# Kernel optimization log

Measured on AMD Instinct MI355X. Metric: run time of the kernel, lower is better.

Reference implementation:

```python
import jax, jax.numpy as jnp
import numpy as np

THR = 0.5      # span-selection threshold
K_SUBJ = 16    # max subject/object spans kept per sentence (padded)
K_OBJ = 8      # max object spans kept per (subject, relation)

# Greedy threshold-based span pairing: for each start position i with
# start_prob>THR, take the first unused j>=i with end_prob>THR (NMS-like).
# Returns fixed-size padded spans [K,2] (int32) and a validity mask [K].
def greedy_spans(sp, ep, K):
    S = sp.shape[0]
    idxs = jnp.arange(S, dtype=jnp.int32)
    def step(carry, i):
        used, count, spans, valid = carry
        gate = sp[i] > THR
        cand = (ep > THR) & (~used) & (idxs >= i)
        has = jnp.any(cand)
        j = jnp.argmax(cand).astype(jnp.int32)  # first True
        found = gate & has
        slot = jnp.minimum(count, K - 1)
        write = found & (count < K)
        pair = jnp.where(write, jnp.stack([i, j]).astype(jnp.int32), spans[slot])
        spans = spans.at[slot].set(pair)
        valid = valid.at[slot].set(valid[slot] | write)
        used = used.at[j].set(used[j] | found)
        count = count + found.astype(jnp.int32)
        return (used, count, spans, valid), None
    init = (jnp.zeros(S, bool), jnp.int32(0),
            jnp.zeros((K, 2), jnp.int32), jnp.zeros(K, bool))
    (_, _, spans, valid), _ = jax.lax.scan(step, init, idxs)
    return spans, valid


def _model(token_embs, hg, rel_embs, b_rel_transe, head_w, head_b,
           Wmats, Wbias, rproj_w, rproj_b, V_w, V_b):
    # head_w/head_b order: 0 start_subj, 1 end_subj, 2 b_start_obj, 3 b_end_obj,
    #                      4 start_obj, 5 end_obj, 6 b_start_subj, 7 b_end_subj
    # Wmats/Wbias order:   0 W_s, 1 W_r, 2 W_g, 3 W_x, 4 W_r_b, 5 W_g_b, 6 W_x_b, 7 W_x2
    sig = jax.nn.sigmoid
    head = lambda x, i: sig(x @ head_w[i] + head_b[i])        # H->1 sigmoid head
    lin = lambda x, i: x @ Wmats[i].T + Wbias[i]              # H->H linear

    # ---- first-level span scores + greedy extraction (forward & backward) ----
    sub_sp, sub_ep = head(token_embs, 0), head(token_embs, 1)   # [B,S]
    bob_sp, bob_ep = head(token_embs, 2), head(token_embs, 3)
    g = jax.vmap(lambda a, b: greedy_spans(a, b, K_SUBJ))
    subj_spans, subj_valid = g(sub_sp, sub_ep)                  # [B,K,2],[B,K]
    b_subj_spans, b_subj_valid = g(bob_sp, bob_ep)

    def gather(tok_b, spans, valid):  # mean of start/end token embeddings
        e = (tok_b[spans[:, 0]] + tok_b[spans[:, 1]]) * 0.5
        return e * valid[:, None].astype(tok_b.dtype)
    s_k = jax.vmap(gather)(token_embs, subj_spans, subj_valid)      # [B,K,H]
    b_s_k = jax.vmap(gather)(token_embs, b_subj_spans, b_subj_valid)
    s_k_w = lin(s_k, 0) * subj_valid[..., None]                     # W_s + mask
    b_s_k_w = lin(b_s_k, 0) * b_subj_valid[..., None]

    # ---- relation-aware attention context C = sum_s A[b,s,r] * x[b,s] ----
    b_rel = b_rel_transe @ rproj_w.T + rproj_b                      # r_proj
    def attend(rels, ir, ig, ix):
        e = jnp.tanh(lin(token_embs, ix)[:, :, None, :]             # [B,S,1,H]
                     + lin(hg, ig)[:, None, None, :]                # [B,1,1,H]
                     + lin(rels, ir)[None, None, :, :])             # [1,1,R,H]
        v = e @ V_w + V_b[0]                                        # [B,S,R]
        A = jax.nn.softmax(v, axis=1)                               # over seq
        return jnp.einsum('bsr,bsh->brh', A, token_embs)            # [B,R,H]
    C = attend(rel_embs, 1, 2, 3)
    b_C = attend(b_rel, 4, 5, 6)

    # Heads are linear, so distribute w over the sum instead of
    # materializing the [B,S,K,R,H] tensor.
    tok_mix = token_embs + lin(token_embs, 7)
    def pair_probs(Cmat, skw, i):
        t_tok = tok_mix @ head_w[i]                                 # [B,S]
        t_sub = skw @ head_w[i]                                     # [B,K]
        t_rel = Cmat @ head_w[i]                                    # [B,R]
        return sig(t_tok[:, :, None, None] + t_sub[:, None, :, None]
                   + t_rel[:, None, None, :] + head_b[i])           # [B,S,K,R]
    obj_sp, obj_ep = pair_probs(C, s_k_w, 4), pair_probs(C, s_k_w, 5)
    bsub_sp, bsub_ep = pair_probs(b_C, b_s_k_w, 6), pair_probs(b_C, b_s_k_w, 7)

    # ---- greedy object-span extraction per (batch, subject, relation) ----
    def triples(sp4, ep4, subj_ok):
        B_, S_, K_, R_ = sp4.shape
        fsp = sp4.transpose(0, 2, 3, 1).reshape(-1, S_)
        fep = ep4.transpose(0, 2, 3, 1).reshape(-1, S_)
        spans, valid = jax.vmap(lambda a, b: greedy_spans(a, b, K_OBJ))(fsp, fep)
        spans = spans.reshape(B_, K_, R_, K_OBJ, 2)
        valid = valid.reshape(B_, K_, R_, K_OBJ) & subj_ok[:, :, None, None]
        return spans, valid
    f_spans, f_valid = triples(obj_sp, obj_ep, subj_valid)
    bw_spans, bw_valid = triples(bsub_sp, bsub_ep, b_subj_valid)

    probs = jnp.stack([obj_sp, obj_ep, bsub_sp, bsub_ep])           # [4,B,S,K,R]
    return (probs, subj_spans, subj_valid, b_subj_spans, b_subj_valid,
            f_spans, f_valid, bw_spans, bw_valid)


def setup_inputs() -> dict:
    key = jax.random.key(0)
    ks = jax.random.split(key, 12)
    B, S, H, R, T = 8, 256, 768, 40, 80
    sc = H ** -0.5
    return {
        'token_embs': jax.random.normal(ks[0], (B, S, H), jnp.float32),
        'hg': jax.random.normal(ks[1], (B, H), jnp.float32),
        'rel_embs': jax.random.normal(ks[2], (R, H), jnp.float32),
        'b_rel_transe': jax.random.normal(ks[3], (R, T), jnp.float32),
        'head_w': jax.random.normal(ks[4], (8, H), jnp.float32) * sc,
        'head_b': jax.random.normal(ks[5], (8,), jnp.float32) * 0.1,
        'Wmats': jax.random.normal(ks[6], (8, H, H), jnp.float32) * sc,
        'Wbias': jax.random.normal(ks[7], (8, H), jnp.float32) * 0.02,
        'rproj_w': jax.random.normal(ks[8], (H, T), jnp.float32) * (T ** -0.5),
        'rproj_b': jax.random.normal(ks[9], (H,), jnp.float32) * 0.02,
        'V_w': jax.random.normal(ks[10], (H,), jnp.float32) * sc,
        'V_b': jax.random.normal(ks[11], (1,), jnp.float32) * 0.1,
    }


def reference(token_embs, hg, rel_embs, b_rel_transe, head_w, head_b,
              Wmats, Wbias, rproj_w, rproj_b, V_w, V_b):
    return _model(token_embs, hg, rel_embs, b_rel_transe, head_w, head_b,
                  Wmats, Wbias, rproj_w, rproj_b, V_w, V_b)
```

## Files before the change

kernel.cpp:

```cpp
#include <hip/hip_runtime.h>
#include <hip/hip_bf16.h>
#include <stdint.h>

#define Bc 8
#define Sc 256
#define Hc 768
#define Rc 40
#define Tc 80
#define KSc 16
#define KOc 8

#define OUT_SSP 5242880
#define OUT_SVA 5243136
#define OUT_BSP 5243264
#define OUT_BVA 5243520
#define OUT_FSP 5243648
#define OUT_FVA 5325568
#define OUT_WSP 5366528
#define OUT_WVA 5448448

#define CM_PS (16 * Rc * Hc)
#define BSH (Bc * Sc * Hc)

__device__ inline double wave_reduce_d(double v) {
#pragma unroll
  for (int o = 32; o; o >>= 1) v += __shfl_down(v, o, 64);
  return v;
}
__device__ inline float wave_reduce_f(float v) {
#pragma unroll
  for (int o = 32; o; o >>= 1) v += __shfl_down(v, o, 64);
  return v;
}

__global__ __launch_bounds__(256) void k_l03(const float* __restrict__ x,
                                             const float* __restrict__ head_w,
                                             const float* __restrict__ head_b,
                                             float* __restrict__ l03) {
  int bs = blockIdx.x * 4 + (threadIdx.x >> 6);
  int lane = threadIdx.x & 63;
  if (bs >= Bc * Sc) return;
  const float* xr = x + (size_t)bs * Hc;
  double acc[4] = {0.0, 0.0, 0.0, 0.0};
  for (int h = lane; h < Hc; h += 64) {
    double xv = (double)xr[h];
    acc[0] += xv * (double)head_w[h];
    acc[1] += xv * (double)head_w[Hc + h];
    acc[2] += xv * (double)head_w[2 * Hc + h];
    acc[3] += xv * (double)head_w[3 * Hc + h];
  }
#pragma unroll
  for (int i = 0; i < 4; ++i) {
    double a = wave_reduce_d(acc[i]);
    if (lane == 0) l03[i * (Bc * Sc) + bs] = (float)(a + (double)head_b[i]);
  }
}

__device__ inline int find_first(const uint64_t* epm, const uint64_t* used, int i) {
  int wi = i >> 6;
  uint64_t m = epm[wi] & ~used[wi] & (~0ull << (i & 63));
  if (m) return (wi << 6) + (__ffsll((unsigned long long)m) - 1);
  for (int w = wi + 1; w < 4; ++w) {
    uint64_t mm = epm[w] & ~used[w];
    if (mm) return (w << 6) + (__ffsll((unsigned long long)mm) - 1);
  }
  return -1;
}

__global__ __launch_bounds__(64) void k_greedy1(const float* __restrict__ l03,
                                                int* __restrict__ spans1, int* __restrict__ valid1,
                                                float* __restrict__ out) {
  int t = blockIdx.x;
  int dir = t >> 3, b = t & 7;
  int lane = threadIdx.x;
  const float* sp = l03 + (dir * 2) * (Bc * Sc) + b * Sc;
  const float* ep = sp + Bc * Sc;
  uint64_t spm[4], epm[4];
#pragma unroll
  for (int w = 0; w < 4; ++w) {
    spm[w] = __ballot(sp[w * 64 + lane] > 0.f);
    epm[w] = __ballot(ep[w * 64 + lane] > 0.f);
  }
  __shared__ int ssp0[KSc], ssp1[KSc], sva[KSc];
  if (lane < KSc) { ssp0[lane] = 0; ssp1[lane] = 0; sva[lane] = 0; }
  __syncthreads();
  if (lane == 0) {
    uint64_t used[4] = {0, 0, 0, 0};
    int cnt = 0;
#pragma unroll
    for (int w = 0; w < 4; ++w) {
      uint64_t g = spm[w];
      while (g) {
        int bit = __ffsll((unsigned long long)g) - 1;
        g &= g - 1;
        int i = w * 64 + bit;
        int j = find_first(epm, used, i);
        if (j < 0) continue;
        used[j >> 6] |= (1ull << (j & 63));
        if (cnt < KSc) { ssp0[cnt] = i; ssp1[cnt] = j; sva[cnt] = 1; }
        cnt++;
      }
    }
  }
  __syncthreads();
  int base = (dir * Bc + b) * KSc;
  float* osp = out + (dir ? OUT_BSP : OUT_SSP) + b * KSc * 2;
  float* ova = out + (dir ? OUT_BVA : OUT_SVA) + b * KSc;
  if (lane < KSc) {
    spans1[(base + lane) * 2] = ssp0[lane];
    spans1[(base + lane) * 2 + 1] = ssp1[lane];
    valid1[base + lane] = sva[lane];
    osp[lane * 2] = (float)ssp0[lane];
    osp[lane * 2 + 1] = (float)ssp1[lane];
    ova[lane] = (float)sva[lane];
  }
}

__global__ __launch_bounds__(256) void k_prep(const float* __restrict__ brt,
                                              const float* __restrict__ rw,
                                              const float* __restrict__ rb,
                                              const float* __restrict__ Wmats,
                                              const float* __restrict__ head_w,
                                              const float* __restrict__ x,
                                              const int* __restrict__ spans1,
                                              float* __restrict__ brel,
                                              double* __restrict__ hv,
                                              float* __restrict__ eb) {
  int bb = blockIdx.x;
  int tid = threadIdx.x;
  if (bb < 12) {
    int idx = bb * 256 + tid;
    int i = idx / Hc, j = idx % Hc;
    const float* h4 = head_w + (4 + i) * Hc;
    const float* W7 = Wmats + (size_t)7 * Hc * Hc;
    double acc = (double)h4[j];
    for (int hh = 0; hh < Hc; ++hh)
      acc += (double)W7[(size_t)hh * Hc + j] * (double)h4[hh];
    hv[idx] = acc;
  } else if (bb < 132) {
    int idx = (bb - 12) * 256 + tid;
    int r = idx / Hc, h = idx % Hc;
    float acc = rb[h];
    const float* a = brt + r * Tc;
    const float* w = rw + (size_t)h * Tc;
    for (int t = 0; t < Tc; ++t) acc = fmaf(a[t], w[t], acc);
    brel[idx] = acc;
  } else {
    int row = bb - 132;
    int b = (row / KSc) % Bc;
    int s0 = spans1[row * 2], s1 = spans1[row * 2 + 1];
    const float* x0 = x + ((size_t)b * Sc + s0) * Hc;
    const float* x1 = x + ((size_t)b * Sc + s1) * Hc;
    float* er = eb + (size_t)row * Hc;
    for (int h = tid; h < Hc; h += 256) er[h] = 0.5f * (x0[h] + x1[h]);
  }
}

__global__ __launch_bounds__(256) void k_skw(const float* __restrict__ eb,
                                             const float* __restrict__ Wmats,
                                             const float* __restrict__ Wbias,
                                             const int* __restrict__ valid1,
                                             float* __restrict__ skw) {
  int m0 = blockIdx.y * 32;
  int n0 = blockIdx.x * 64;
  __shared__ float Asl[32][36];
  __shared__ float Bsl[32][68];
  int tid = threadIdx.x;
  int arow = tid >> 3, acol = (tid & 7) << 2;
  int brow = tid >> 2, bcol = (tid & 3) << 2;
  int txi = tid & 15, tyi = tid >> 4;
  const float* ap = eb + (size_t)(m0 + arow) * Hc + acol;
  const float* bp = Wmats + (size_t)(n0 + brow) * Hc + bcol;
  int nb = n0 + txi * 4;
  float4 bias = *(const float4*)&Wbias[nb];
  float acc[2][4];
#pragma unroll
  for (int i = 0; i < 2; ++i) { acc[i][0] = bias.x; acc[i][1] = bias.y; acc[i][2] = bias.z; acc[i][3] = bias.w; }
  for (int k0 = 0; k0 < Hc; k0 += 32) {
    float4 av = *(const float4*)(ap + k0);
    float4 b0 = *(const float4*)(bp + k0);
    float4 b1 = *(const float4*)(bp + k0 + 16);
    __syncthreads();
    Asl[acol + 0][arow] = av.x; Asl[acol + 1][arow] = av.y; Asl[acol + 2][arow] = av.z; Asl[acol + 3][arow] = av.w;
    Bsl[bcol + 0][brow] = b0.x; Bsl[bcol + 1][brow] = b0.y; Bsl[bcol + 2][brow] = b0.z; Bsl[bcol + 3][brow] = b0.w;
    Bsl[bcol + 16][brow] = b1.x; Bsl[bcol + 17][brow] = b1.y; Bsl[bcol + 18][brow] = b1.z; Bsl[bcol + 19][brow] = b1.w;
    __syncthreads();
#pragma unroll
    for (int kk = 0; kk < 32; ++kk) {
      float a0 = Asl[kk][tyi * 2], a1 = Asl[kk][tyi * 2 + 1];
      float4 b = *(const float4*)&Bsl[kk][txi * 4];
      acc[0][0] = fmaf(a0, b.x, acc[0][0]); acc[0][1] = fmaf(a0, b.y, acc[0][1]);
      acc[0][2] = fmaf(a0, b.z, acc[0][2]); acc[0][3] = fmaf(a0, b.w, acc[0][3]);
      acc[1][0] = fmaf(a1, b.x, acc[1][0]); acc[1][1] = fmaf(a1, b.y, acc[1][1]);
      acc[1][2] = fmaf(a1, b.z, acc[1][2]); acc[1][3] = fmaf(a1, b.w, acc[1][3]);
    }
  }
  int m_ = m0 + tyi * 2;
#pragma unroll
  for (int i = 0; i < 2; ++i) {
    int v = valid1[m_ + i];
    float4 o;
    o.x = v ? acc[i][0] : 0.f; o.y = v ? acc[i][1] : 0.f;
    o.z = v ? acc[i][2] : 0.f; o.w = v ? acc[i][3] : 0.f;
    *(float4*)&skw[(size_t)(m_ + i) * Hc + nb] = o;
  }
}

__global__ __launch_bounds__(256) void k_tgtr(const float* __restrict__ hg,
                                              const float* __restrict__ rel,
                                              const float* __restrict__ brel,
                                              const float* __restrict__ Wmats,
                                              const float* __restrict__ Wbias,
                                              float* __restrict__ tg,
                                              float* __restrict__ tr) {
  int grp = blockIdx.z;
  const float* Asrc; int M; int wsel; float* dst;
  if (grp == 0)      { Asrc = hg;   M = 8;  wsel = 2; dst = tg; }
  else if (grp == 1) { Asrc = hg;   M = 8;  wsel = 5; dst = tg + 8 * Hc; }
  else if (grp == 2) { Asrc = rel;  M = 40; wsel = 1; dst = tr; }
  else               { Asrc = brel; M = 40; wsel = 4; dst = tr + 40 * Hc; }
  int m0 = blockIdx.y * 32;
  if (m0 >= M) return;
  int n0 = blockIdx.x * 64;
  const float* W = Wmats + (size_t)wsel * Hc * Hc;
  const float* bias = Wbias + wsel * Hc;
  __shared__ float Asl[32][36];
  __shared__ float Bsl[32][68];
  int tid = threadIdx.x;
  int arow = tid >> 3, acol = (tid & 7) << 2;
  int brow = tid >> 2, bcol = (tid & 3) << 2;
  int txi = tid & 15, tyi = tid >> 4;
  int ar = m0 + arow;
  const float* ap = Asrc + (size_t)(ar < M ? ar : 0) * Hc + acol;
  const float* bp = W + (size_t)(n0 + brow) * Hc + bcol;
  int nb = n0 + txi * 4;
  float4 bv = *(const float4*)&bias[nb];
  float acc[2][4];
#pragma unroll
  for (int i = 0; i < 2; ++i) { acc[i][0] = bv.x; acc[i][1] = bv.y; acc[i][2] = bv.z; acc[i][3] = bv.w; }
  for (int k0 = 0; k0 < Hc; k0 += 32) {
    float4 av = *(const float4*)(ap + k0);
    float4 b0 = *(const float4*)(bp + k0);
    float4 b1 = *(const float4*)(bp + k0 + 16);
    __syncthreads();
    Asl[acol + 0][arow] = av.x; Asl[acol + 1][arow] = av.y; Asl[acol + 2][arow] = av.z; Asl[acol + 3][arow] = av.w;
    Bsl[bcol + 0][brow] = b0.x; Bsl[bcol + 1][brow] = b0.y; Bsl[bcol + 2][brow] = b0.z; Bsl[bcol + 3][brow] = b0.w;
    Bsl[bcol + 16][brow] = b1.x; Bsl[bcol + 17][brow] = b1.y; Bsl[bcol + 18][brow] = b1.z; Bsl[bcol + 19][brow] = b1.w;
    __syncthreads();
#pragma unroll
    for (int kk = 0; kk < 32; ++kk) {
      float a0 = Asl[kk][tyi * 2], a1 = Asl[kk][tyi * 2 + 1];
      float4 b = *(const float4*)&Bsl[kk][txi * 4];
      acc[0][0] = fmaf(a0, b.x, acc[0][0]); acc[0][1] = fmaf(a0, b.y, acc[0][1]);
      acc[0][2] = fmaf(a0, b.z, acc[0][2]); acc[0][3] = fmaf(a0, b.w, acc[0][3]);
      acc[1][0] = fmaf(a1, b.x, acc[1][0]); acc[1][1] = fmaf(a1, b.y, acc[1][1]);
      acc[1][2] = fmaf(a1, b.z, acc[1][2]); acc[1][3] = fmaf(a1, b.w, acc[1][3]);
    }
  }
  int m_ = m0 + tyi * 2;
#pragma unroll
  for (int i = 0; i < 2; ++i) {
    if (m_ + i < M) {
      float4 o; o.x = acc[i][0]; o.y = acc[i][1]; o.z = acc[i][2]; o.w = acc[i][3];
      *(float4*)&dst[(size_t)(m_ + i) * Hc + nb] = o;
    }
  }
}

#define BM 64
#define BN 64
#define BKK 32
#define LDP 68
__global__ __launch_bounds__(256) void k_tx(const float* __restrict__ x,
                                            const float* __restrict__ Wmats,
                                            const float* __restrict__ Wbias,
                                            float* __restrict__ txo) {
  int dir = blockIdx.z;
  const float* W = Wmats + (size_t)(dir ? 6 : 3) * Hc * Hc;
  const float* bias = Wbias + (dir ? 6 : 3) * Hc;
  float* outp = txo + (size_t)dir * BSH;
  int m0 = blockIdx.y * BM;
  int n0 = blockIdx.x * BN;
  __shared__ float Asl[BKK][LDP];
  __shared__ float Bsl[BKK][LDP];
  int tid = threadIdx.x;
  int lr = tid >> 2;
  int lc = (tid & 3) << 2;
  int txi = tid & 15, tyi = tid >> 4;
  const float* xp = x + (size_t)(m0 + lr) * Hc + lc;
  const float* wp = W + (size_t)(n0 + lr) * Hc + lc;
  float4 a0 = *(const float4*)(xp);
  float4 a1 = *(const float4*)(xp + 16);
  float4 b0 = *(const float4*)(wp);
  float4 b1 = *(const float4*)(wp + 16);
  float acc[4][4] = {};
  for (int k0 = 0; k0 < Hc; k0 += BKK) {
    __syncthreads();
    Asl[lc + 0][lr] = a0.x; Asl[lc + 1][lr] = a0.y; Asl[lc + 2][lr] = a0.z; Asl[lc + 3][lr] = a0.w;
    Asl[lc + 16][lr] = a1.x; Asl[lc + 17][lr] = a1.y; Asl[lc + 18][lr] = a1.z; Asl[lc + 19][lr] = a1.w;
    Bsl[lc + 0][lr] = b0.x; Bsl[lc + 1][lr] = b0.y; Bsl[lc + 2][lr] = b0.z; Bsl[lc + 3][lr] = b0.w;
    Bsl[lc + 16][lr] = b1.x; Bsl[lc + 17][lr] = b1.y; Bsl[lc + 18][lr] = b1.z; Bsl[lc + 19][lr] = b1.w;
    __syncthreads();
    if (k0 + BKK < Hc) {
      a0 = *(const float4*)(xp + k0 + BKK);
      a1 = *(const float4*)(xp + k0 + BKK + 16);
      b0 = *(const float4*)(wp + k0 + BKK);
      b1 = *(const float4*)(wp + k0 + BKK + 16);
    }
#pragma unroll
    for (int kk = 0; kk < BKK; ++kk) {
      float4 a = *(const float4*)&Asl[kk][tyi * 4];
      float4 b = *(const float4*)&Bsl[kk][txi * 4];
      acc[0][0] = fmaf(a.x, b.x, acc[0][0]); acc[0][1] = fmaf(a.x, b.y, acc[0][1]);
      acc[0][2] = fmaf(a.x, b.z, acc[0][2]); acc[0][3] = fmaf(a.x, b.w, acc[0][3]);
      acc[1][0] = fmaf(a.y, b.x, acc[1][0]); acc[1][1] = fmaf(a.y, b.y, acc[1][1]);
      acc[1][2] = fmaf(a.y, b.z, acc[1][2]); acc[1][3] = fmaf(a.y, b.w, acc[1][3]);
      acc[2][0] = fmaf(a.z, b.x, acc[2][0]); acc[2][1] = fmaf(a.z, b.y, acc[2][1]);
      acc[2][2] = fmaf(a.z, b.z, acc[2][2]); acc[2][3] = fmaf(a.z, b.w, acc[2][3]);
      acc[3][0] = fmaf(a.w, b.x, acc[3][0]); acc[3][1] = fmaf(a.w, b.y, acc[3][1]);
      acc[3][2] = fmaf(a.w, b.z, acc[3][2]); acc[3][3] = fmaf(a.w, b.w, acc[3][3]);
    }
  }
  int nb = n0 + txi * 4;
  float4 bb = *(const float4*)&bias[nb];
#pragma unroll
  for (int i2 = 0; i2 < 4; ++i2) {
    float4 o;
    o.x = acc[i2][0] + bb.x; o.y = acc[i2][1] + bb.y;
    o.z = acc[i2][2] + bb.z; o.w = acc[i2][3] + bb.w;
    *(float4*)&outp[(size_t)(m0 + tyi * 4 + i2) * Hc + nb] = o;
  }
}

__global__ __launch_bounds__(256) void k_v(const float* __restrict__ txo,
                                           const float* __restrict__ tg,
                                           const float* __restrict__ tr,
                                           const float* __restrict__ Vw,
                                           const float* __restrict__ Vb,
                                           float* __restrict__ va) {
  const float Cl = 2.8853900817779268f;
  int id = blockIdx.x;
  int dir = id >> 10;
  int rem = id & 1023;
  int rhalf = rem & 1;
  int bs0 = (rem >> 1) * 4;
  int b = bs0 >> 8;
  int tid = threadIdx.x;
  int wv = tid >> 6, lane = tid & 63;
  const float* tgr = tg + (dir * Bc + b) * Hc;
  float xt[4][12], vw[12];
#pragma unroll
  for (int u = 0; u < 12; ++u) {
    int h = lane + 64 * u;
    vw[u] = Vw[h];
    float tgv = tgr[h];
#pragma unroll
    for (int si = 0; si < 4; ++si)
      xt[si][u] = (txo[((size_t)dir * (Bc * Sc) + bs0 + si) * Hc + h] + tgv) * Cl;
  }
  float vb0 = Vb[0];
  for (int q = 0; q < 5; ++q) {
    int r = rhalf * 20 + wv * 5 + q;
    const float* trr = tr + ((size_t)dir * Rc + r) * Hc + lane;
    float p0 = 0.f, p1 = 0.f, p2 = 0.f, p3 = 0.f;
#pragma unroll
    for (int u = 0; u < 12; ++u) {
      float t = trr[64 * u] * Cl;
      float e0 = __builtin_amdgcn_exp2f(xt[0][u] + t);
      float e1 = __builtin_amdgcn_exp2f(xt[1][u] + t);
      float e2 = __builtin_amdgcn_exp2f(xt[2][u] + t);
      float e3 = __builtin_amdgcn_exp2f(xt[3][u] + t);
      p0 = fmaf(fmaf(-2.f, __builtin_amdgcn_rcpf(e0 + 1.f), 1.f), vw[u], p0);
      p1 = fmaf(fmaf(-2.f, __builtin_amdgcn_rcpf(e1 + 1.f), 1.f), vw[u], p1);
      p2 = fmaf(fmaf(-2.f, __builtin_amdgcn_rcpf(e2 + 1.f), 1.f), vw[u], p2);
      p3 = fmaf(fmaf(-2.f, __builtin_amdgcn_rcpf(e3 + 1.f), 1.f), vw[u], p3);
    }
    p0 = wave_reduce_f(p0); p1 = wave_reduce_f(p1);
    p2 = wave_reduce_f(p2); p3 = wave_reduce_f(p3);
    if (lane == 0) {
      size_t base = ((size_t)dir * (Bc * Sc) + bs0) * Rc + r;
      va[base] = p0 + vb0;
      va[base + Rc] = p1 + vb0;
      va[base + 2 * Rc] = p2 + vb0;
      va[base + 3 * Rc] = p3 + vb0;
    }
  }
}

__global__ __launch_bounds__(256) void k_softmax(float* __restrict__ va) {
  int id = blockIdx.x;
  int dir = id / (Bc * Rc); int rem = id % (Bc * Rc);
  int b = rem / Rc; int r = rem % Rc;
  int s = threadIdx.x;
  float* base = va + (((size_t)dir * Bc + b) * Sc) * Rc + r;
  float v = base[(size_t)s * Rc];
  __shared__ float red[8];
  float m = v;
#pragma unroll
  for (int o = 32; o; o >>= 1) m = fmaxf(m, __shfl_xor(m, o, 64));
  if ((s & 63) == 0) red[s >> 6] = m;
  __syncthreads();
  if (s == 0) red[4] = fmaxf(fmaxf(red[0], red[1]), fmaxf(red[2], red[3]));
  __syncthreads();
  m = red[4];
  float e = expf(v - m);
  float t = e;
#pragma unroll
  for (int o = 32; o; o >>= 1) t += __shfl_xor(t, o, 64);
  __syncthreads();
  if ((s & 63) == 0) red[s >> 6] = t;
  __syncthreads();
  if (s == 0) red[4] = red[0] + red[1] + red[2] + red[3];
  __syncthreads();
  base[(size_t)s * Rc] = e / red[4];
}

__global__ __launch_bounds__(256, 1) void k_C(const float* __restrict__ va,
                                              const float* __restrict__ x,
                                              float* __restrict__ Cm4) {
  int id = blockIdx.x;
  int p = id & 3;
  int g = id >> 2;
  int b = g & 7;
  __shared__ float As_[64 * Rc];
  int tid = threadIdx.x;
  const float* vab = va + ((size_t)g * Sc + p * 64) * Rc;
  for (int idx = tid; idx < 64 * Rc; idx += 256) As_[idx] = vab[idx];
  __syncthreads();
  const float* xb = x + ((size_t)b * Sc + p * 64) * Hc;
  float acc[3][Rc];
#pragma unroll
  for (int j = 0; j < 3; ++j)
#pragma unroll
    for (int r = 0; r < Rc; ++r) acc[j][r] = 0.f;
  for (int s = 0; s < 64; ++s) {
    float xv0 = xb[(size_t)s * Hc + tid];
    float xv1 = xb[(size_t)s * Hc + 256 + tid];
    float xv2 = xb[(size_t)s * Hc + 512 + tid];
#pragma unroll
    for (int q = 0; q < 10; ++q) {
      float4 a4 = *(const float4*)&As_[s * Rc + q * 4];
      acc[0][q * 4 + 0] = fmaf(a4.x, xv0, acc[0][q * 4 + 0]);
      acc[0][q * 4 + 1] = fmaf(a4.y, xv0, acc[0][q * 4 + 1]);
      acc[0][q * 4 + 2] = fmaf(a4.z, xv0, acc[0][q * 4 + 2]);
      acc[0][q * 4 + 3] = fmaf(a4.w, xv0, acc[0][q * 4 + 3]);
      acc[1][q * 4 + 0] = fmaf(a4.x, xv1, acc[1][q * 4 + 0]);
      acc[1][q * 4 + 1] = fmaf(a4.y, xv1, acc[1][q * 4 + 1]);
      acc[1][q * 4 + 2] = fmaf(a4.z, xv1, acc[1][q * 4 + 2]);
      acc[1][q * 4 + 3] = fmaf(a4.w, xv1, acc[1][q * 4 + 3]);
      acc[2][q * 4 + 0] = fmaf(a4.x, xv2, acc[2][q * 4 + 0]);
      acc[2][q * 4 + 1] = fmaf(a4.y, xv2, acc[2][q * 4 + 1]);
      acc[2][q * 4 + 2] = fmaf(a4.z, xv2, acc[2][q * 4 + 2]);
      acc[2][q * 4 + 3] = fmaf(a4.w, xv2, acc[2][q * 4 + 3]);
    }
  }
#pragma unroll
  for (int r = 0; r < Rc; ++r) {
    size_t base = ((size_t)(p * 16 + g) * Rc + r) * Hc + tid;
    Cm4[base] = acc[0][r];
    Cm4[base + 256] = acc[1][r];
    Cm4[base + 512] = acc[2][r];
  }
}

__global__ __launch_bounds__(256) void k_tt(const float* __restrict__ x,
                                            const double* __restrict__ hv,
                                            double* __restrict__ tt) {
  int bs = blockIdx.x * 4 + (threadIdx.x >> 6);
  int lane = threadIdx.x & 63;
  if (bs >= Bc * Sc) return;
  const float* xr = x + (size_t)bs * Hc;
  double acc[4] = {0.0, 0.0, 0.0, 0.0};
  for (int h = lane; h < Hc; h += 64) {
    double xv = (double)xr[h];
    acc[0] += xv * hv[h];
    acc[1] += xv * hv[Hc + h];
    acc[2] += xv * hv[2 * Hc + h];
    acc[3] += xv * hv[3 * Hc + h];
  }
#pragma unroll
  for (int i = 0; i < 4; ++i) {
    double a = wave_reduce_d(acc[i]);
    if (lane == 0) tt[i * (Bc * Sc) + bs] = a;
  }
}

__global__ __launch_bounds__(256) void k_tsc(const float* __restrict__ skw,
                                             const float* __restrict__ Cm4,
                                             const float* __restrict__ head_w,
                                             const float* __restrict__ Wbias,
                                             double* __restrict__ ts,
                                             double* __restrict__ trl,
                                             double* __restrict__ c4) {
  int wave = blockIdx.x * 4 + (threadIdx.x >> 6);
  int lane = threadIdx.x & 63;
  const float* src; const float* w; double* dst;
  bool partial4 = false;
  if (wave < 512) {
    int p = wave >> 7, rem = wave & 127;
    int b = rem >> 4, k = rem & 15, dir = p >> 1;
    src = skw + (((size_t)(dir * Bc + b)) * KSc + k) * Hc;
    w = head_w + (4 + p) * Hc;
    dst = ts + (p * Bc + b) * KSc + k;
  } else if (wave < 1792) {
    int q = wave - 512;
    int p = q / 320, rem = q % 320;
    int b = rem / Rc, r = rem % Rc, dir = p >> 1;
    src = Cm4 + ((size_t)(dir * Bc + b) * Rc + r) * Hc;
    w = head_w + (4 + p) * Hc;
    dst = trl + (p * Bc + b) * Rc + r;
    partial4 = true;
  } else if (wave < 1796) {
    int p = wave - 1792;
    src = Wbias + 7 * Hc;
    w = head_w + (4 + p) * Hc;
    dst = c4 + p;
  } else return;
  double acc = 0.0;
  if (partial4) {
    for (int h = lane; h < Hc; h += 64) {
      double cs = (double)src[h] + (double)src[h + CM_PS] +
                  (double)src[h + 2 * CM_PS] + (double)src[h + 3 * CM_PS];
      acc += cs * (double)w[h];
    }
  } else {
    for (int h = lane; h < Hc; h += 64) acc += (double)src[h] * (double)w[h];
  }
  acc = wave_reduce_d(acc);
  if (lane == 0) *dst = acc;
}

__global__ __launch_bounds__(256) void k_probs(const double* __restrict__ tt,
                                               const double* __restrict__ ts,
                                               const double* __restrict__ trl,
                                               const double* __restrict__ c4,
                                               const float* __restrict__ head_b,
                                               float* __restrict__ out) {
  int id = blockIdx.x;
  int b = id >> 8, s = id & 255;
  (void)s;
  __shared__ double tsb[4][KSc];
  __shared__ double trb[4][Rc];
  __shared__ double basep[4];
  int tid = threadIdx.x;
  if (tid < 64) { int p = tid >> 4, k = tid & 15; tsb[p][k] = ts[(p * Bc + b) * KSc + k]; }
  if (tid < 160) { int p = tid / Rc, r = tid % Rc; trb[p][r] = trl[(p * Bc + b) * Rc + r]; }
  if (tid < 4) basep[tid] = tt[tid * (Bc * Sc) + id] + c4[tid] + (double)head_b[4 + tid];
  __syncthreads();
#pragma unroll
  for (int p = 0; p < 4; ++p) {
    double base = basep[p];
    float* op = out + ((size_t)(p * Bc) * Sc + id) * (KSc * Rc);
    for (int kr = tid; kr < KSc * Rc; kr += 256) {
      int k = kr / Rc, r = kr - k * Rc;
      double l = base + tsb[p][k] + trb[p][r];
      op[kr] = 1.f / (1.f + expf(-(float)l));
    }
  }
}

__global__ __launch_bounds__(256) void k_greedy2(const double* __restrict__ tt,
                                                 const double* __restrict__ ts,
                                                 const double* __restrict__ trl,
                                                 const double* __restrict__ c4,
                                                 const float* __restrict__ head_b,
                                                 const int* __restrict__ valid1,
                                                 float* __restrict__ out) {
  int gid = blockIdx.x * blockDim.x + threadIdx.x;
  if (gid >= 2 * Bc * KSc * Rc) return;
  int dir = gid / (Bc * KSc * Rc);
  int rem = gid % (Bc * KSc * Rc);
  int b = rem / (KSc * Rc);
  int kr = rem % (KSc * Rc);
  int k = kr / Rc, r = kr % Rc;
  int p0 = dir * 2, p1 = p0 + 1;
  double off0 = ts[(p0 * Bc + b) * KSc + k] + trl[(p0 * Bc + b) * Rc + r] + c4[p0] + (double)head_b[4 + p0];
  double off1 = ts[(p1 * Bc + b) * KSc + k] + trl[(p1 * Bc + b) * Rc + r] + c4[p1] + (double)head_b[4 + p1];
  const double* t0 = tt + p0 * (Bc * Sc) + b * Sc;
  const double* t1 = tt + p1 * (Bc * Sc) + b * Sc;
  uint64_t spm[4], epm[4], used[4] = {0, 0, 0, 0};
#pragma unroll
  for (int w = 0; w < 4; ++w) {
    uint64_t ms = 0, me = 0;
    for (int bit = 0; bit < 64; ++bit) {
      int s = w * 64 + bit;
      if (t0[s] + off0 > 0.0) ms |= (1ull << bit);
      if (t1[s] + off1 > 0.0) me |= (1ull << bit);
    }
    spm[w] = ms; epm[w] = me;
  }
  float* osp = out + (dir ? OUT_WSP : OUT_FSP) + (size_t)rem * KOc * 2;
  float* ova = out + (dir ? OUT_WVA : OUT_FVA) + (size_t)rem * KOc;
  for (int o = 0; o < KOc; ++o) { osp[o * 2] = 0.f; osp[o * 2 + 1] = 0.f; ova[o] = 0.f; }
  float sval = valid1[(dir * Bc + b) * KSc + k] ? 1.f : 0.f;
  int cnt = 0;
  for (int w = 0; w < 4; ++w) {
    uint64_t g = spm[w];
    while (g) {
      int bit = __ffsll((unsigned long long)g) - 1;
      g &= g - 1;
      int i = w * 64 + bit;
      int j = find_first(epm, used, i);
      if (j < 0) continue;
      used[j >> 6] |= (1ull << (j & 63));
      if (cnt < KOc) { osp[cnt * 2] = (float)i; osp[cnt * 2 + 1] = (float)j; ova[cnt] = sval; }
      cnt++;
    }
  }
}

extern "C" void kernel_launch(void* const* d_in, const int* in_sizes, int n_in,
                              void* d_out, int out_size, void* d_ws, size_t ws_size,
                              hipStream_t stream) {
  (void)in_sizes; (void)n_in; (void)out_size; (void)ws_size;
  const float* x = (const float*)d_in[0];
  const float* hg = (const float*)d_in[1];
  const float* rel = (const float*)d_in[2];
  const float* brt = (const float*)d_in[3];
  const float* head_w = (const float*)d_in[4];
  const float* head_b = (const float*)d_in[5];
  const float* Wmats = (const float*)d_in[6];
  const float* Wbias = (const float*)d_in[7];
  const float* rproj_w = (const float*)d_in[8];
  const float* rproj_b = (const float*)d_in[9];
  const float* Vw = (const float*)d_in[10];
  const float* Vb = (const float*)d_in[11];
  float* out = (float*)d_out;
  char* ws = (char*)d_ws;

  double* hv  = (double*)(ws + 0);
  double* c4  = (double*)(ws + 24576);
  double* tt  = (double*)(ws + 24608);
  double* ts  = (double*)(ws + 90144);
  double* trl = (double*)(ws + 94240);
  float* l03  = (float*)(ws + 104480);
  float* brel = (float*)(ws + 137248);
  float* tg   = (float*)(ws + 260128);
  float* tr   = (float*)(ws + 309280);
  float* txb  = (float*)(ws + 555040);
  float* va   = (float*)(ws + 13137952);
  float* skw  = (float*)(ws + 15759392);
  int* spans1 = (int*)(ws + 16545824);
  int* valid1 = (int*)(ws + 16547872);
  float* eb   = txb;
  float* Cm4  = txb;

  k_l03<<<512, 256, 0, stream>>>(x, head_w, head_b, l03);
  k_greedy1<<<16, 64, 0, stream>>>(l03, spans1, valid1, out);
  k_prep<<<388, 256, 0, stream>>>(brt, rproj_w, rproj_b, Wmats, head_w, x, spans1, brel, hv, eb);
  k_skw<<<dim3(12, 8), 256, 0, stream>>>(eb, Wmats, Wbias, valid1, skw);
  k_tgtr<<<dim3(12, 2, 4), 256, 0, stream>>>(hg, rel, brel, Wmats, Wbias, tg, tr);
  k_tx<<<dim3(12, 32, 2), 256, 0, stream>>>(x, Wmats, Wbias, txb);
  k_v<<<2048, 256, 0, stream>>>(txb, tg, tr, Vw, Vb, va);
  k_softmax<<<640, 256, 0, stream>>>(va);
  k_C<<<64, 256, 0, stream>>>(va, x, Cm4);
  k_tt<<<512, 256, 0, stream>>>(x, hv, tt);
  k_tsc<<<449, 256, 0, stream>>>(skw, Cm4, head_w, Wbias, ts, trl, c4);
  k_probs<<<2048, 256, 0, stream>>>(tt, ts, trl, c4, head_b, out);
  k_greedy2<<<40, 256, 0, stream>>>(tt, ts, trl, c4, head_b, valid1, out);
}
```

Baseline: 353.2 us.

## Retile tx GEMM to 128x128, fuse tt into l03 pass, split k_C over relations

The tx GEMM moves from 64x64 to 128x128 tiles with an 8x8 register micro-tile per thread. This raises arithmetic intensity, and the bias add is moved into k_v. The hv/brel precompute is split into its own kernel that runs first, so the tt dot products can share the x read with the l03 head scores. The span gather becomes a separate kernel. k_C is split across two relation halves to double the block count and cut per-thread accumulator registers. The trade-offs are fewer blocks for the GEMM (192), possibly higher register pressure, and one extra kernel launch.

```diff
diff --git a/kernel.cpp b/kernel.cpp
--- a/kernel.cpp
+++ b/kernel.cpp
@@ -33,26 +33,66 @@
   return v;
 }
 
-__global__ __launch_bounds__(256) void k_l03(const float* __restrict__ x,
-                                             const float* __restrict__ head_w,
-                                             const float* __restrict__ head_b,
-                                             float* __restrict__ l03) {
+__global__ __launch_bounds__(256) void k_prep0(const float* __restrict__ brt,
+                                               const float* __restrict__ rw,
+                                               const float* __restrict__ rb,
+                                               const float* __restrict__ Wmats,
+                                               const float* __restrict__ head_w,
+                                               float* __restrict__ brel,
+                                               double* __restrict__ hv) {
+  int bb = blockIdx.x;
+  int tid = threadIdx.x;
+  if (bb < 12) {
+    int idx = bb * 256 + tid;
+    int i = idx / Hc, j = idx % Hc;
+    const float* h4 = head_w + (4 + i) * Hc;
+    const float* W7 = Wmats + (size_t)7 * Hc * Hc;
+    double acc = (double)h4[j];
+    for (int hh = 0; hh < Hc; ++hh)
+      acc += (double)W7[(size_t)hh * Hc + j] * (double)h4[hh];
+    hv[idx] = acc;
+  } else {
+    int idx = (bb - 12) * 256 + tid;
+    int r = idx / Hc, h = idx % Hc;
+    float acc = rb[h];
+    const float* a = brt + r * Tc;
+    const float* w = rw + (size_t)h * Tc;
+    for (int t = 0; t < Tc; ++t) acc = fmaf(a[t], w[t], acc);
+    brel[idx] = acc;
+  }
+}
+
+__global__ __launch_bounds__(256) void k_l03tt(const float* __restrict__ x,
+                                               const float* __restrict__ head_w,
+                                               const float* __restrict__ head_b,
+                                               const double* __restrict__ hv,
+                                               float* __restrict__ l03,
+                                               double* __restrict__ tt) {
   int bs = blockIdx.x * 4 + (threadIdx.x >> 6);
   int lane = threadIdx.x & 63;
   if (bs >= Bc * Sc) return;
   const float* xr = x + (size_t)bs * Hc;
-  double acc[4] = {0.0, 0.0, 0.0, 0.0};
+  double acc[8] = {0, 0, 0, 0, 0, 0, 0, 0};
   for (int h = lane; h < Hc; h += 64) {
     double xv = (double)xr[h];
     acc[0] += xv * (double)head_w[h];
     acc[1] += xv * (double)head_w[Hc + h];
     acc[2] += xv * (double)head_w[2 * Hc + h];
     acc[3] += xv * (double)head_w[3 * Hc + h];
+    acc[4] += xv * hv[h];
+    acc[5] += xv * hv[Hc + h];
+    acc[6] += xv * hv[2 * Hc + h];
+    acc[7] += xv * hv[3 * Hc + h];
   }
 #pragma unroll
   for (int i = 0; i < 4; ++i) {
     double a = wave_reduce_d(acc[i]);
     if (lane == 0) l03[i * (Bc * Sc) + bs] = (float)(a + (double)head_b[i]);
+  }
+#pragma unroll
+  for (int i = 0; i < 4; ++i) {
+    double a = wave_reduce_d(acc[4 + i]);
+    if (lane == 0) tt[i * (Bc * Sc) + bs] = a;
   }
 }
 
@@ -116,44 +156,16 @@
   }
 }
 
-__global__ __launch_bounds__(256) void k_prep(const float* __restrict__ brt,
-                                              const float* __restrict__ rw,
-                                              const float* __restrict__ rb,
-                                              const float* __restrict__ Wmats,
-                                              const float* __restrict__ head_w,
-                                              const float* __restrict__ x,
-                                              const int* __restrict__ spans1,
-                                              float* __restrict__ brel,
-                                              double* __restrict__ hv,
-                                              float* __restrict__ eb) {
-  int bb = blockIdx.x;
-  int tid = threadIdx.x;
-  if (bb < 12) {
-    int idx = bb * 256 + tid;
-    int i = idx / Hc, j = idx % Hc;
-    const float* h4 = head_w + (4 + i) * Hc;
-    const float* W7 = Wmats + (size_t)7 * Hc * Hc;
-    double acc = (double)h4[j];
-    for (int hh = 0; hh < Hc; ++hh)
-      acc += (double)W7[(size_t)hh * Hc + j] * (double)h4[hh];
-    hv[idx] = acc;
-  } else if (bb < 132) {
-    int idx = (bb - 12) * 256 + tid;
-    int r = idx / Hc, h = idx % Hc;
-    float acc = rb[h];
-    const float* a = brt + r * Tc;
-    const float* w = rw + (size_t)h * Tc;
-    for (int t = 0; t < Tc; ++t) acc = fmaf(a[t], w[t], acc);
-    brel[idx] = acc;
-  } else {
-    int row = bb - 132;
-    int b = (row / KSc) % Bc;
-    int s0 = spans1[row * 2], s1 = spans1[row * 2 + 1];
-    const float* x0 = x + ((size_t)b * Sc + s0) * Hc;
-    const float* x1 = x + ((size_t)b * Sc + s1) * Hc;
-    float* er = eb + (size_t)row * Hc;
-    for (int h = tid; h < Hc; h += 256) er[h] = 0.5f * (x0[h] + x1[h]);
-  }
+__global__ __launch_bounds__(256) void k_egather(const float* __restrict__ x,
+                                                 const int* __restrict__ spans1,
+                                                 float* __restrict__ eb) {
+  int row = blockIdx.x;
+  int b = (row / KSc) % Bc;
+  int s0 = spans1[row * 2], s1 = spans1[row * 2 + 1];
+  const float* x0 = x + ((size_t)b * Sc + s0) * Hc;
+  const float* x1 = x + ((size_t)b * Sc + s1) * Hc;
+  float* er = eb + (size_t)row * Hc;
+  for (int h = threadIdx.x; h < Hc; h += 256) er[h] = 0.5f * (x0[h] + x1[h]);
 }
 
 __global__ __launch_bounds__(256) void k_skw(const float* __restrict__ eb,
@@ -267,72 +279,73 @@
   }
 }
 
-#define BM 64
-#define BN 64
-#define BKK 32
-#define LDP 68
-__global__ __launch_bounds__(256) void k_tx(const float* __restrict__ x,
-                                            const float* __restrict__ Wmats,
-                                            const float* __restrict__ Wbias,
-                                            float* __restrict__ txo) {
+__global__ __launch_bounds__(256) void k_tx2(const float* __restrict__ x,
+                                             const float* __restrict__ Wmats,
+                                             float* __restrict__ txo) {
   int dir = blockIdx.z;
   const float* W = Wmats + (size_t)(dir ? 6 : 3) * Hc * Hc;
-  const float* bias = Wbias + (dir ? 6 : 3) * Hc;
   float* outp = txo + (size_t)dir * BSH;
-  int m0 = blockIdx.y * BM;
-  int n0 = blockIdx.x * BN;
-  __shared__ float Asl[BKK][LDP];
-  __shared__ float Bsl[BKK][LDP];
+  int m0 = blockIdx.y * 128;
+  int n0 = blockIdx.x * 128;
+  __shared__ float Asl[16 * 192];
+  __shared__ float Bsl[16 * 192];
   int tid = threadIdx.x;
-  int lr = tid >> 2;
-  int lc = (tid & 3) << 2;
   int txi = tid & 15, tyi = tid >> 4;
-  const float* xp = x + (size_t)(m0 + lr) * Hc + lc;
-  const float* wp = W + (size_t)(n0 + lr) * Hc + lc;
+  int sr = tid >> 1, skq = (tid & 1) * 8;
+  const float* xp = x + (size_t)(m0 + sr) * Hc + skq;
+  const float* wp = W + (size_t)(n0 + sr) * Hc + skq;
+  float* awp = &Asl[(sr >> 3) * 12 + (sr & 7)];
+  float* bwp = &Bsl[(sr >> 3) * 12 + (sr & 7)];
+  const float* arp = &Asl[tyi * 12];
+  const float* brp = &Bsl[txi * 12];
   float4 a0 = *(const float4*)(xp);
-  float4 a1 = *(const float4*)(xp + 16);
+  float4 a1 = *(const float4*)(xp + 4);
   float4 b0 = *(const float4*)(wp);
-  float4 b1 = *(const float4*)(wp + 16);
-  float acc[4][4] = {};
-  for (int k0 = 0; k0 < Hc; k0 += BKK) {
+  float4 b1 = *(const float4*)(wp + 4);
+  float acc[8][8] = {};
+  const int NT = 48;
+  for (int kt = 0; kt < NT; ++kt) {
     __syncthreads();
-    Asl[lc + 0][lr] = a0.x; Asl[lc + 1][lr] = a0.y; Asl[lc + 2][lr] = a0.z; Asl[lc + 3][lr] = a0.w;
-    Asl[lc + 16][lr] = a1.x; Asl[lc + 17][lr] = a1.y; Asl[lc + 18][lr] = a1.z; Asl[lc + 19][lr] = a1.w;
-    Bsl[lc + 0][lr] = b0.x; Bsl[lc + 1][lr] = b0.y; Bsl[lc + 2][lr] = b0.z; Bsl[lc + 3][lr] = b0.w;
-    Bsl[lc + 16][lr] = b1.x; Bsl[lc + 17][lr] = b1.y; Bsl[lc + 18][lr] = b1.z; Bsl[lc + 19][lr] = b1.w;
+    awp[(skq + 0) * 192] = a0.x; awp[(skq + 1) * 192] = a0.y; awp[(skq + 2) * 192] = a0.z; awp[(skq + 3) * 192] = a0.w;
+    awp[(skq + 4) * 192] = a1.x; awp[(skq + 5) * 192] = a1.y; awp[(skq + 6) * 192] = a1.z; awp[(skq + 7) * 192] = a1.w;
+    bwp[(skq + 0) * 192] = b0.x; bwp[(skq + 1) * 192] = b0.y; bwp[(skq + 2) * 192] = b0.z; bwp[(skq + 3) * 192] = b0.w;
+    bwp[(skq + 4) * 192] = b1.x; bwp[(skq + 5) * 192] = b1.y; bwp[(skq + 6) * 192] = b1.z; bwp[(skq + 7) * 192] = b1.w;
     __syncthreads();
-    if (k0 + BKK < Hc) {
-      a0 = *(const float4*)(xp + k0 + BKK);
-      a1 = *(const float4*)(xp + k0 + BKK + 16);
-      b0 = *(const float4*)(wp + k0 + BKK);
-      b1 = *(const float4*)(wp + k0 + BKK + 16);
-    }
-#pragma unroll
-    for (int kk = 0; kk < BKK; ++kk) {
-      float4 a = *(const float4*)&Asl[kk][tyi * 4];
-      float4 b = *(const float4*)&Bsl[kk][txi * 4];
-      acc[0][0] = fmaf(a.x, b.x, acc[0][0]); acc[0][1] = fmaf(a.x, b.y, acc[0][1]);
-      acc[0][2] = fmaf(a.x, b.z, acc[0][2]); acc[0][3] = fmaf(a.x, b.w, acc[0][3]);
-      acc[1][0] = fmaf(a.y, b.x, acc[1][0]); acc[1][1] = fmaf(a.y, b.y, acc[1][1]);
-      acc[1][2] = fmaf(a.y, b.z, acc[1][2]); acc[1][3] = fmaf(a.y, b.w, acc[1][3]);
-      acc[2][0] = fmaf(a.z, b.x, acc[2][0]); acc[2][1] = fmaf(a.z, b.y, acc[2][1]);
-      acc[2][2] = fmaf(a.z, b.z, acc[2][2]); acc[2][3] = fmaf(a.z, b.w, acc[2][3]);
-      acc[3][0] = fmaf(a.w, b.x, acc[3][0]); acc[3][1] = fmaf(a.w, b.y, acc[3][1]);
-      acc[3][2] = fmaf(a.w, b.z, acc[3][2]); acc[3][3] = fmaf(a.w, b.w, acc[3][3]);
-    }
-  }
-  int nb = n0 + txi * 4;
-  float4 bb = *(const float4*)&bias[nb];
-#pragma unroll
-  for (int i2 = 0; i2 < 4; ++i2) {
-    float4 o;
-    o.x = acc[i2][0] + bb.x; o.y = acc[i2][1] + bb.y;
-    o.z = acc[i2][2] + bb.z; o.w = acc[i2][3] + bb.w;
-    *(float4*)&outp[(size_t)(m0 + tyi * 4 + i2) * Hc + nb] = o;
+    if (kt + 1 < NT) {
+      int ko = (kt + 1) * 16;
+      a0 = *(const float4*)(xp + ko);
+      a1 = *(const float4*)(xp + ko + 4);
+      b0 = *(const float4*)(wp + ko);
+      b1 = *(const float4*)(wp + ko + 4);
+    }
+#pragma unroll
+    for (int kk = 0; kk < 16; ++kk) {
+      float4 A0 = *(const float4*)&arp[kk * 192];
+      float4 A1 = *(const float4*)&arp[kk * 192 + 4];
+      float4 B0 = *(const float4*)&brp[kk * 192];
+      float4 B1 = *(const float4*)&brp[kk * 192 + 4];
+      float aF[8] = {A0.x, A0.y, A0.z, A0.w, A1.x, A1.y, A1.z, A1.w};
+      float bF[8] = {B0.x, B0.y, B0.z, B0.w, B1.x, B1.y, B1.z, B1.w};
+#pragma unroll
+      for (int i = 0; i < 8; ++i)
+#pragma unroll
+        for (int j = 0; j < 8; ++j)
+          acc[i][j] = fmaf(aF[i], bF[j], acc[i][j]);
+    }
+  }
+#pragma unroll
+  for (int i = 0; i < 8; ++i) {
+    float* orow = outp + (size_t)(m0 + tyi * 8 + i) * Hc + n0 + txi * 8;
+    float4 o0, o1;
+    o0.x = acc[i][0]; o0.y = acc[i][1]; o0.z = acc[i][2]; o0.w = acc[i][3];
+    o1.x = acc[i][4]; o1.y = acc[i][5]; o1.z = acc[i][6]; o1.w = acc[i][7];
+    *(float4*)orow = o0;
+    *(float4*)(orow + 4) = o1;
   }
 }
 
 __global__ __launch_bounds__(256) void k_v(const float* __restrict__ txo,
+                                           const float* __restrict__ Wbias,
                                            const float* __restrict__ tg,
                                            const float* __restrict__ tr,
                                            const float* __restrict__ Vw,
@@ -348,15 +361,19 @@
   int tid = threadIdx.x;
   int wv = tid >> 6, lane = tid & 63;
   const float* tgr = tg + (dir * Bc + b) * Hc;
+  const float* wb = Wbias + (dir ? 6 : 3) * Hc;
   float xt[4][12], vw[12];
 #pragma unroll
   for (int u = 0; u < 12; ++u) {
     int h = lane + 64 * u;
     vw[u] = Vw[h];
+    float wbv = wb[h];
     float tgv = tgr[h];
 #pragma unroll
-    for (int si = 0; si < 4; ++si)
-      xt[si][u] = (txo[((size_t)dir * (Bc * Sc) + bs0 + si) * Hc + h] + tgv) * Cl;
+    for (int si = 0; si < 4; ++si) {
+      float tv = txo[((size_t)dir * (Bc * Sc) + bs0 + si) * Hc + h] + wbv;
+      xt[si][u] = (tv + tgv) * Cl;
+    }
   }
   float vb0 = Vb[0];
   for (int q = 0; q < 5; ++q) {
@@ -419,8 +436,9 @@
                                               const float* __restrict__ x,
                                               float* __restrict__ Cm4) {
   int id = blockIdx.x;
-  int p = id & 3;
-  int g = id >> 2;
+  int rr = id & 1;
+  int p = (id >> 1) & 3;
+  int g = id >> 3;
   int b = g & 7;
   __shared__ float As_[64 * Rc];
   int tid = threadIdx.x;
@@ -428,18 +446,19 @@
   for (int idx = tid; idx < 64 * Rc; idx += 256) As_[idx] = vab[idx];
   __syncthreads();
   const float* xb = x + ((size_t)b * Sc + p * 64) * Hc;
-  float acc[3][Rc];
+  float acc[3][20];
 #pragma unroll
   for (int j = 0; j < 3; ++j)
 #pragma unroll
-    for (int r = 0; r < Rc; ++r) acc[j][r] = 0.f;
+    for (int r = 0; r < 20; ++r) acc[j][r] = 0.f;
+  int rbase = rr * 20;
   for (int s = 0; s < 64; ++s) {
     float xv0 = xb[(size_t)s * Hc + tid];
     float xv1 = xb[(size_t)s * Hc + 256 + tid];
     float xv2 = xb[(size_t)s * Hc + 512 + tid];
 #pragma unroll
-    for (int q = 0; q < 10; ++q) {
-      float4 a4 = *(const float4*)&As_[s * Rc + q * 4];
+    for (int q = 0; q < 5; ++q) {
+      float4 a4 = *(const float4*)&As_[s * Rc + rbase + q * 4];
       acc[0][q * 4 + 0] = fmaf(a4.x, xv0, acc[0][q * 4 + 0]);
       acc[0][q * 4 + 1] = fmaf(a4.y, xv0, acc[0][q * 4 + 1]);
       acc[0][q * 4 + 2] = fmaf(a4.z, xv0, acc[0][q * 4 + 2]);
@@ -455,33 +474,11 @@
     }
   }
 #pragma unroll
-  for (int r = 0; r < Rc; ++r) {
-    size_t base = ((size_t)(p * 16 + g) * Rc + r) * Hc + tid;
+  for (int r = 0; r < 20; ++r) {
+    size_t base = ((size_t)(p * 16 + g) * Rc + rbase + r) * Hc + tid;
     Cm4[base] = acc[0][r];
     Cm4[base + 256] = acc[1][r];
     Cm4[base + 512] = acc[2][r];
-  }
-}
-
-__global__ __launch_bounds__(256) void k_tt(const float* __restrict__ x,
-                                            const double* __restrict__ hv,
-                                            double* __restrict__ tt) {
-  int bs = blockIdx.x * 4 + (threadIdx.x >> 6);
-  int lane = threadIdx.x & 63;
-  if (bs >= Bc * Sc) return;
-  const float* xr = x + (size_t)bs * Hc;
-  double acc[4] = {0.0, 0.0, 0.0, 0.0};
-  for (int h = lane; h < Hc; h += 64) {
-    double xv = (double)xr[h];
-    acc[0] += xv * hv[h];
-    acc[1] += xv * hv[Hc + h];
-    acc[2] += xv * hv[2 * Hc + h];
-    acc[3] += xv * hv[3 * Hc + h];
-  }
-#pragma unroll
-  for (int i = 0; i < 4; ++i) {
-    double a = wave_reduce_d(acc[i]);
-    if (lane == 0) tt[i * (Bc * Sc) + bs] = a;
   }
 }
 
@@ -645,16 +642,16 @@
   float* eb   = txb;
   float* Cm4  = txb;
 
-  k_l03<<<512, 256, 0, stream>>>(x, head_w, head_b, l03);
+  k_prep0<<<132, 256, 0, stream>>>(brt, rproj_w, rproj_b, Wmats, head_w, brel, hv);
+  k_l03tt<<<512, 256, 0, stream>>>(x, head_w, head_b, hv, l03, tt);
   k_greedy1<<<16, 64, 0, stream>>>(l03, spans1, valid1, out);
-  k_prep<<<388, 256, 0, stream>>>(brt, rproj_w, rproj_b, Wmats, head_w, x, spans1, brel, hv, eb);
+  k_egather<<<256, 256, 0, stream>>>(x, spans1, eb);
   k_skw<<<dim3(12, 8), 256, 0, stream>>>(eb, Wmats, Wbias, valid1, skw);
   k_tgtr<<<dim3(12, 2, 4), 256, 0, stream>>>(hg, rel, brel, Wmats, Wbias, tg, tr);
-  k_tx<<<dim3(12, 32, 2), 256, 0, stream>>>(x, Wmats, Wbias, txb);
-  k_v<<<2048, 256, 0, stream>>>(txb, tg, tr, Vw, Vb, va);
+  k_tx2<<<dim3(6, 16, 2), 256, 0, stream>>>(x, Wmats, txb);
+  k_v<<<2048, 256, 0, stream>>>(txb, Wbias, tg, tr, Vw, Vb, va);
   k_softmax<<<640, 256, 0, stream>>>(va);
-  k_C<<<64, 256, 0, stream>>>(va, x, Cm4);
-  k_tt<<<512, 256, 0, stream>>>(x, hv, tt);
+  k_C<<<128, 256, 0, stream>>>(va, x, Cm4);
   k_tsc<<<449, 256, 0, stream>>>(skw, Cm4, head_w, Wbias, ts, trl, c4);
   k_probs<<<2048, 256, 0, stream>>>(tt, ts, trl, c4, head_b, out);
   k_greedy2<<<40, 256, 0, stream>>>(tt, ts, trl, c4, head_b, valid1, out);
```

Result: slower. 361.2 us (+2.2%).
